# Kernel tuning notes

Measured on AMD Instinct MI355X. Metric: run time of the kernel, lower is better.

## Reference

```python
import jax, jax.numpy as jnp
import numpy as np

TOP_K = 2
NORM_TOPK_PROB = True


def setup_inputs() -> dict:
    key = jax.random.key(0)
    k1, k2, k3 = jax.random.split(key, 3)
    B, S, H, E = 4, 2048, 2048, 8
    hidden_states = jax.random.normal(k1, (B, S, H), dtype=jnp.float32)
    gate_w = jax.random.normal(k2, (E, H), dtype=jnp.float32) * 0.02   # nn.Linear weight [E, H]
    expert_w = jax.random.normal(k3, (E, H, H), dtype=jnp.float32) * 0.02  # per-expert Linear weight [H_out, H_in]
    return {"hidden_states": hidden_states, "gate_w": gate_w, "expert_w": expert_w}


def reference(hidden_states, gate_w, expert_w):
    B, S, H = hidden_states.shape
    E = gate_w.shape[0]
    x = hidden_states.reshape(-1, H)                      # [T, H], T = B*S
    T = x.shape[0]

    router_logits = x @ gate_w.T                          # [T, E]
    probs = jax.nn.softmax(router_logits.astype(jnp.float32), axis=-1)
    top_w, top_i = jax.lax.top_k(probs, TOP_K)            # [T, K]
    if NORM_TOPK_PROB:
        top_w = top_w / jnp.sum(top_w, axis=-1, keepdims=True)
    top_w = top_w.astype(x.dtype)

    # dense [T, E] combine weights (scatter of top-k weights)
    w_full = jnp.zeros((T, E), dtype=x.dtype).at[jnp.arange(T)[:, None], top_i].add(top_w)

    # expert_i(x) = x @ W_i.T  (bias-free Linear)
    expert_out = jnp.einsum('th,eoh->eto', x, expert_w)   # [E, T, H]
    out = jnp.einsum('te,eto->to', w_full, expert_out)    # [T, H]

    return out.reshape(B, S, H), router_logits.reshape(B, S, E)
```

## Files before the change

kernel.cpp:

```cpp
#include <hip/hip_runtime.h>
#include <stdint.h>

#define T_TOK 8192
#define HDIM  2048
#define NEXP  8
#define TILE  128
#define BK    64
#define RTOK  32

typedef __bf16 bf16x8 __attribute__((ext_vector_type(8)));
typedef float  f32x4  __attribute__((ext_vector_type(4)));
typedef unsigned short u16;
typedef u16    u16x8  __attribute__((ext_vector_type(8)));

typedef const __attribute__((address_space(1))) void* gptr_t;
typedef __attribute__((address_space(3))) void* lptr_t;

static __device__ __forceinline__ u16 f2bf(float f) {
    union { float f; unsigned u; } v; v.f = f;
    unsigned u = v.u;
    u = (u + 0x7FFFu + ((u >> 16) & 1u)) >> 16;
    return (u16)u;
}

__global__ __launch_bounds__(256) void cvt_kernel(const float* __restrict__ in,
                                                  u16* __restrict__ out, int n8) {
    int i = blockIdx.x * 256 + threadIdx.x;
    if (i >= n8) return;
    const float4* p = (const float4*)in + (size_t)i * 2;
    float4 a = p[0], b = p[1];
    u16x8 r;
    r[0] = f2bf(a.x); r[1] = f2bf(a.y); r[2] = f2bf(a.z); r[3] = f2bf(a.w);
    r[4] = f2bf(b.x); r[5] = f2bf(b.y); r[6] = f2bf(b.z); r[7] = f2bf(b.w);
    ((u16x8*)out)[i] = r;
}

__global__ __launch_bounds__(256) void router_kernel(const float* __restrict__ x,
                                                     const float* __restrict__ gw,
                                                     u16* __restrict__ xb,
                                                     float* __restrict__ logits_out,
                                                     int* __restrict__ cnt,
                                                     int* __restrict__ rows,
                                                     float* __restrict__ wts) {
    __shared__ int   lcnt[NEXP];
    __shared__ int   lbase[NEXP];
    __shared__ int   lrows[NEXP][RTOK];
    __shared__ float lwtsS[NEXP][RTOK];

    int tid  = threadIdx.x;
    int lane = tid & 63;
    int wave = tid >> 6;
    if (tid < NEXP) lcnt[tid] = 0;
    __syncthreads();

    int t0 = blockIdx.x * RTOK + wave * 8;
    const float4* g4 = (const float4*)gw;

    float acc[8][NEXP] = {};
    #pragma unroll
    for (int i = 0; i < HDIM / 4 / 64; i++) {
        int idx = lane + i * 64;
        float4 gv[NEXP];
        #pragma unroll
        for (int e = 0; e < NEXP; e++) gv[e] = g4[e * (HDIM / 4) + idx];
        #pragma unroll
        for (int tk = 0; tk < 8; tk++) {
            int t = t0 + tk;
            float4 xv = ((const float4*)(x + (size_t)t * HDIM))[idx];
            ushort4 h;
            h.x = f2bf(xv.x); h.y = f2bf(xv.y); h.z = f2bf(xv.z); h.w = f2bf(xv.w);
            ((ushort4*)(xb + (size_t)t * HDIM))[idx] = h;
            #pragma unroll
            for (int e = 0; e < NEXP; e++)
                acc[tk][e] += xv.x * gv[e].x + xv.y * gv[e].y +
                              xv.z * gv[e].z + xv.w * gv[e].w;
        }
    }
    #pragma unroll
    for (int tk = 0; tk < 8; tk++)
        #pragma unroll
        for (int e = 0; e < NEXP; e++)
            #pragma unroll
            for (int off = 32; off > 0; off >>= 1)
                acc[tk][e] += __shfl_xor(acc[tk][e], off, 64);

    if (lane == 0) {
        #pragma unroll
        for (int tk = 0; tk < 8; tk++) {
            int t = t0 + tk;
            #pragma unroll
            for (int e = 0; e < NEXP; e++) logits_out[(size_t)t * NEXP + e] = acc[tk][e];
            int e0 = 0;
            #pragma unroll
            for (int e = 1; e < NEXP; e++) if (acc[tk][e] > acc[tk][e0]) e0 = e;
            int e1 = (e0 == 0) ? 1 : 0;
            #pragma unroll
            for (int e = 0; e < NEXP; e++)
                if (e != e0 && acc[tk][e] > acc[tk][e1]) e1 = e;
            float w0 = 1.0f / (1.0f + expf(acc[tk][e1] - acc[tk][e0]));
            int p0 = atomicAdd(&lcnt[e0], 1);
            lrows[e0][p0] = t * 2;     lwtsS[e0][p0] = w0;
            int p1 = atomicAdd(&lcnt[e1], 1);
            lrows[e1][p1] = t * 2 + 1; lwtsS[e1][p1] = 1.0f - w0;
        }
    }
    __syncthreads();
    if (tid < NEXP) lbase[tid] = atomicAdd(&cnt[tid], lcnt[tid]);
    __syncthreads();
    int e = tid >> 5, j = tid & 31;
    if (j < lcnt[e]) {
        int b = lbase[e] + j;
        rows[e * T_TOK + b] = lrows[e][j];
        wts[e * T_TOK + b]  = lwtsS[e][j];
    }
}

__global__ __launch_bounds__(256) void moe_gemm(const u16* __restrict__ xb,
                                                const u16* __restrict__ wb,
                                                const int* __restrict__ cnt,
                                                const int* __restrict__ rows,
                                                const float* __restrict__ wts,
                                                u16* __restrict__ cbuf) {
    int p  = blockIdx.x;
    int xc = p & 7;
    int q  = p >> 3;
    int rt = q & 63;
    int g  = (q >> 6) * 8 + xc;
    int e  = g >> 4;
    int nb = (g & 15) * TILE;

    int count = cnt[e];
    int rowBase = rt * TILE;
    if (rowBase >= count) return;

    const u16*   W     = wb  + (size_t)e * HDIM * HDIM;
    const int*   rlist = rows + e * T_TOK;
    const float* wlist = wts  + e * T_TOK;

    __shared__ u16 As[2][TILE * BK];
    __shared__ u16 Bs[2][TILE * BK];

    int tid  = threadIdx.x;
    int lane = tid & 63;
    int wave = tid >> 6;
    int wr = wave >> 1, wc = wave & 1;

    const u16* a_src[4];
    const u16* b_src[4];
    #pragma unroll
    for (int pp = 0; pp < 4; pp++) {
        int row  = (tid >> 3) + pp * 32;
        int clog = (tid & 7) ^ (row & 7);
        int tok  = rlist[min(rowBase + row, count - 1)] >> 1;
        a_src[pp] = xb + (size_t)tok * HDIM + clog * 8;
        b_src[pp] = W + (size_t)(nb + row) * HDIM + clog * 8;
    }
    int wslot = (tid & ~63);

    auto stage = [&](u16* A_lds, u16* B_lds, int kb) {
        #pragma unroll
        for (int pp = 0; pp < 4; pp++) {
            __builtin_amdgcn_global_load_lds((gptr_t)(a_src[pp] + kb),
                                             (lptr_t)(A_lds + (pp * 256 + wslot) * 8),
                                             16, 0, 0);
            __builtin_amdgcn_global_load_lds((gptr_t)(b_src[pp] + kb),
                                             (lptr_t)(B_lds + (pp * 256 + wslot) * 8),
                                             16, 0, 0);
        }
    };

    int lrow = lane & 15;
    int kq   = lane >> 4;
    int mloc[4], nloc[4];
    #pragma unroll
    for (int i = 0; i < 4; i++) {
        mloc[i] = wr * 64 + i * 16 + lrow;
        nloc[i] = wc * 64 + i * 16 + lrow;
    }

    f32x4 acc[4][4] = {};

    auto compute = [&](const u16* A_lds, const u16* B_lds) {
        #pragma unroll
        for (int s = 0; s < 2; s++) {
            int chunk = s * 4 + kq;
            bf16x8 a[4], b[4];
            #pragma unroll
            for (int i = 0; i < 4; i++) {
                int aslot = (mloc[i] << 3) | (chunk ^ (mloc[i] & 7));
                int bslot = (nloc[i] << 3) | (chunk ^ (nloc[i] & 7));
                a[i] = *(const bf16x8*)(A_lds + aslot * 8);
                b[i] = *(const bf16x8*)(B_lds + bslot * 8);
            }
            #pragma unroll
            for (int mt = 0; mt < 4; mt++)
                #pragma unroll
                for (int nt = 0; nt < 4; nt++)
                    acc[mt][nt] = __builtin_amdgcn_mfma_f32_16x16x32_bf16(
                                      a[mt], b[nt], acc[mt][nt], 0, 0, 0);
        }
    };

    stage(As[0], Bs[0], 0);
    stage(As[1], Bs[1], BK);

    for (int kb = 0; kb < HDIM - 2 * BK; kb += 2 * BK) {
        asm volatile("s_waitcnt vmcnt(8)" ::: "memory");
        __builtin_amdgcn_sched_barrier(0);
        __builtin_amdgcn_s_barrier();
        compute(As[0], Bs[0]);
        __builtin_amdgcn_sched_barrier(0);
        __builtin_amdgcn_s_barrier();
        stage(As[0], Bs[0], kb + 2 * BK);

        asm volatile("s_waitcnt vmcnt(8)" ::: "memory");
        __builtin_amdgcn_sched_barrier(0);
        __builtin_amdgcn_s_barrier();
        compute(As[1], Bs[1]);
        __builtin_amdgcn_sched_barrier(0);
        __builtin_amdgcn_s_barrier();
        stage(As[1], Bs[1], kb + 3 * BK);
    }
    asm volatile("s_waitcnt vmcnt(8)" ::: "memory");
    __builtin_amdgcn_sched_barrier(0);
    __builtin_amdgcn_s_barrier();
    compute(As[0], Bs[0]);
    asm volatile("s_waitcnt vmcnt(0)" ::: "memory");
    __builtin_amdgcn_sched_barrier(0);
    __builtin_amdgcn_s_barrier();
    compute(As[1], Bs[1]);

    int srow = (lane >> 4) * 4;
    #pragma unroll
    for (int mt = 0; mt < 4; mt++) {
        #pragma unroll
        for (int r = 0; r < 4; r++) {
            int row = rowBase + wr * 64 + mt * 16 + srow + r;
            if (row < count) {
                int   slot = rlist[row];
                float wgt  = wlist[row];
                u16* crow = cbuf + (size_t)slot * HDIM;
                #pragma unroll
                for (int nt = 0; nt < 4; nt++) {
                    int col = nb + wc * 64 + nt * 16 + lrow;
                    crow[col] = f2bf(wgt * acc[mt][nt][r]);
                }
            }
        }
    }
}

__global__ __launch_bounds__(256) void combine_kernel(const u16* __restrict__ cbuf,
                                                      float* __restrict__ out) {
    int t  = blockIdx.x;
    int c8 = threadIdx.x;
    u16x8 a = ((const u16x8*)(cbuf + (size_t)(t * 2)     * HDIM))[c8];
    u16x8 b = ((const u16x8*)(cbuf + (size_t)(t * 2 + 1) * HDIM))[c8];
    float4 o[2];
    #pragma unroll
    for (int j = 0; j < 8; j++) {
        union { unsigned u; float f; } va, vb;
        va.u = (unsigned)a[j] << 16;
        vb.u = (unsigned)b[j] << 16;
        ((float*)o)[j] = va.f + vb.f;
    }
    float4* op = (float4*)(out + (size_t)t * HDIM + c8 * 8);
    op[0] = o[0];
    op[1] = o[1];
}

extern "C" void kernel_launch(void* const* d_in, const int* in_sizes, int n_in,
                              void* d_out, int out_size, void* d_ws, size_t ws_size,
                              hipStream_t stream) {
    const float* x  = (const float*)d_in[0];
    const float* gw = (const float*)d_in[1];
    const float* ew = (const float*)d_in[2];
    float* out    = (float*)d_out;
    float* logits = out + (size_t)T_TOK * HDIM;

    char* ws = (char*)d_ws;
    int*   cnt  = (int*)ws;
    int*   rows = (int*)(ws + 1024);
    float* wts  = (float*)(ws + 1024 + 262144);
    u16*   xb   = (u16*)(ws + 1024 + 2 * 262144);
    u16*   wb   = xb + (size_t)T_TOK * HDIM;
    u16*   cbuf = wb + (size_t)NEXP * HDIM * HDIM;

    hipMemsetAsync(cnt, 0, NEXP * sizeof(int), stream);

    int nw8 = NEXP * HDIM * HDIM / 8;
    cvt_kernel<<<(nw8 + 255) / 256, 256, 0, stream>>>(ew, wb, nw8);

    router_kernel<<<T_TOK / RTOK, 256, 0, stream>>>(x, gw, xb, logits, cnt, rows, wts);

    moe_gemm<<<NEXP * 64 * 16, 256, 0, stream>>>(xb, wb, cnt, rows, wts, cbuf);

    combine_kernel<<<T_TOK, 256, 0, stream>>>(cbuf, out);
}
```

Baseline: 560.9 us.

## Merge weight conversion into router kernel and remap GEMM block order

```diff
diff --git a/kernel.cpp b/kernel.cpp
--- a/kernel.cpp
+++ b/kernel.cpp
@@ -7,6 +7,7 @@
 #define TILE  128
 #define BK    64
 #define RTOK  32
+#define NRBLK (T_TOK / RTOK)
 
 typedef __bf16 bf16x8 __attribute__((ext_vector_type(8)));
 typedef float  f32x4  __attribute__((ext_vector_type(4)));
@@ -23,31 +24,33 @@
     return (u16)u;
 }
 
-__global__ __launch_bounds__(256) void cvt_kernel(const float* __restrict__ in,
-                                                  u16* __restrict__ out, int n8) {
-    int i = blockIdx.x * 256 + threadIdx.x;
-    if (i >= n8) return;
-    const float4* p = (const float4*)in + (size_t)i * 2;
-    float4 a = p[0], b = p[1];
-    u16x8 r;
-    r[0] = f2bf(a.x); r[1] = f2bf(a.y); r[2] = f2bf(a.z); r[3] = f2bf(a.w);
-    r[4] = f2bf(b.x); r[5] = f2bf(b.y); r[6] = f2bf(b.z); r[7] = f2bf(b.w);
-    ((u16x8*)out)[i] = r;
-}
-
-__global__ __launch_bounds__(256) void router_kernel(const float* __restrict__ x,
-                                                     const float* __restrict__ gw,
-                                                     u16* __restrict__ xb,
-                                                     float* __restrict__ logits_out,
-                                                     int* __restrict__ cnt,
-                                                     int* __restrict__ rows,
-                                                     float* __restrict__ wts) {
+__global__ __launch_bounds__(256) void cvt_router_kernel(const float* __restrict__ x,
+                                                         const float* __restrict__ gw,
+                                                         const float* __restrict__ ew,
+                                                         u16* __restrict__ xb,
+                                                         u16* __restrict__ wb,
+                                                         float* __restrict__ logits_out,
+                                                         int* __restrict__ cnt,
+                                                         int* __restrict__ rows,
+                                                         float* __restrict__ wts) {
     __shared__ int   lcnt[NEXP];
     __shared__ int   lbase[NEXP];
     __shared__ int   lrows[NEXP][RTOK];
     __shared__ float lwtsS[NEXP][RTOK];
 
-    int tid  = threadIdx.x;
+    int tid = threadIdx.x;
+
+    if (blockIdx.x >= NRBLK) {
+        int i = (blockIdx.x - NRBLK) * 256 + tid;
+        const float4* p = (const float4*)ew + (size_t)i * 2;
+        float4 a = p[0], b = p[1];
+        u16x8 r;
+        r[0] = f2bf(a.x); r[1] = f2bf(a.y); r[2] = f2bf(a.z); r[3] = f2bf(a.w);
+        r[4] = f2bf(b.x); r[5] = f2bf(b.y); r[6] = f2bf(b.z); r[7] = f2bf(b.w);
+        ((u16x8*)wb)[i] = r;
+        return;
+    }
+
     int lane = tid & 63;
     int wave = tid >> 6;
     if (tid < NEXP) lcnt[tid] = 0;
@@ -121,13 +124,11 @@
                                                 const int* __restrict__ rows,
                                                 const float* __restrict__ wts,
                                                 u16* __restrict__ cbuf) {
-    int p  = blockIdx.x;
-    int xc = p & 7;
-    int q  = p >> 3;
-    int rt = q & 63;
-    int g  = (q >> 6) * 8 + xc;
-    int e  = g >> 4;
-    int nb = (g & 15) * TILE;
+    int p     = blockIdx.x;
+    int e     = p & 7;
+    int local = p >> 3;
+    int rt    = local >> 4;
+    int nb    = (local & 15) * TILE;
 
     int count = cnt[e];
     int rowBase = rt * TILE;
@@ -289,9 +290,9 @@
     hipMemsetAsync(cnt, 0, NEXP * sizeof(int), stream);
 
     int nw8 = NEXP * HDIM * HDIM / 8;
-    cvt_kernel<<<(nw8 + 255) / 256, 256, 0, stream>>>(ew, wb, nw8);
-
-    router_kernel<<<T_TOK / RTOK, 256, 0, stream>>>(x, gw, xb, logits, cnt, rows, wts);
+    int ncvt = nw8 / 256;
+    cvt_router_kernel<<<NRBLK + ncvt, 256, 0, stream>>>(x, gw, ew, xb, wb,
+                                                        logits, cnt, rows, wts);
 
     moe_gemm<<<NEXP * 64 * 16, 256, 0, stream>>>(xb, wb, cnt, rows, wts, cbuf);
 
```

New measurement: 522.3 us. 1.07x faster.
